# Optimization experiments

Hardware: AMD Instinct MI355X
Metric: run time of the kernel (lower is better)

## Reference

```python
import jax, jax.numpy as jnp
import numpy as np
from jax import lax

# ---- static config (R-C3D TEST cfg) ----
FEAT_STRIDE = 8
SCALES = np.array([2, 4, 5, 6, 8, 9, 10, 12, 14, 16], dtype=np.float32)
NUM_ANCHORS = SCALES.shape[0]  # A = 10
PRE_NMS_TOP_N = 6000
POST_NMS_TOP_N = 300
NMS_THRESH = 0.7
MIN_SIZE = 8.0


def _generate_anchors():
    # matches generate_anchors(base_size=feat_stride, scales): centered temporal windows
    ctr = (FEAT_STRIDE - 1) / 2.0
    ws = SCALES * FEAT_STRIDE
    return np.stack([ctr - 0.5 * (ws - 1.0), ctr + 0.5 * (ws - 1.0)], axis=1).astype(np.float32)  # [A,2]


def setup_inputs() -> dict:
    key = jax.random.key(0)
    k1, k2 = jax.random.split(key)
    B, L = 4, 4096
    scores_in = jax.random.normal(k1, (B, 2 * NUM_ANCHORS, L, 1, 1), dtype=jnp.float32)
    twin_deltas = jax.random.normal(k2, (B, 2 * NUM_ANCHORS, L, 1, 1), dtype=jnp.float32) * 0.1
    return {"scores_in": scores_in, "twin_deltas": twin_deltas}


def _iou_1d(twins):
    # twins: [N,2] inclusive temporal segments (torch-style +1 lengths)
    x1, x2 = twins[:, 0], twins[:, 1]
    length = x2 - x1 + 1.0
    inter = jnp.maximum(0.0, jnp.minimum(x2[:, None], x2[None, :]) - jnp.maximum(x1[:, None], x1[None, :]) + 1.0)
    union = length[:, None] + length[None, :] - inter
    return inter / union


def _nms_keep(iou, thresh):
    # greedy NMS on score-sorted candidates; keep[i] iff no earlier kept j overlaps > thresh
    N = iou.shape[0]
    idx = jnp.arange(N)
    def body(i, keep):
        suppressed = jnp.any(keep & (iou[:, i] > thresh) & (idx < i))
        return keep.at[i].set(~suppressed)
    return lax.fori_loop(0, N, body, jnp.zeros((N,), dtype=bool))


def _forward(scores_in, twin_deltas):
    B = scores_in.shape[0]
    A = NUM_ANCHORS
    L = scores_in.shape[2]
    anchors0 = jnp.asarray(_generate_anchors())  # [A,2]

    # objectness scores: second half of channels
    scores = scores_in[:, A:, :, :, :]  # [B,A,L,1,1]

    # shifted anchors, shift-major / anchor-minor to match (L,H,W,A) flattening
    shifts = jnp.arange(L, dtype=scores_in.dtype) * FEAT_STRIDE  # [L]
    anc = (anchors0[None, :, :] + shifts[:, None, None]).reshape(L * A, 2)  # [K*A,2]

    deltas = jnp.transpose(twin_deltas, (0, 2, 3, 4, 1)).reshape(B, -1, 2)  # [B,K*A,2]
    sc = jnp.transpose(scores, (0, 2, 3, 4, 1)).reshape(B, -1)  # [B,K*A]

    # twin_transform_inv
    widths = anc[:, 1] - anc[:, 0] + 1.0  # [K*A]
    ctr = anc[:, 0] + 0.5 * widths
    pred_ctr = deltas[:, :, 0] * widths[None, :] + ctr[None, :]
    pred_l = jnp.exp(deltas[:, :, 1]) * widths[None, :]
    proposals = jnp.stack([pred_ctr - 0.5 * pred_l, pred_ctr + 0.5 * pred_l], axis=-1)  # [B,K*A,2]

    # clip_twins to [0, L*feat_stride - 1]
    proposals = jnp.clip(proposals, 0.0, L * FEAT_STRIDE - 1.0)

    # filter: zero scores of too-short proposals
    ls = proposals[:, :, 1] - proposals[:, :, 0] + 1.0
    sc = jnp.where(ls < MIN_SIZE, 0.0, sc)

    # sort by score descending, take pre-NMS top-N
    order = jnp.argsort(-sc, axis=1)[:, :PRE_NMS_TOP_N]  # [B,P]
    prop_sorted = jnp.take_along_axis(proposals, order[:, :, None], axis=1)  # [B,P,2]

    def per_image(p):
        iou = _iou_1d(lax.stop_gradient(p))  # NMS decision is non-differentiable (layer propagates no grads via NMS)
        keep = _nms_keep(iou, NMS_THRESH)
        N = p.shape[0]
        # kept indices in sorted order, padded with N
        kept_idx = jnp.sort(jnp.where(keep, jnp.arange(N), N))[:POST_NMS_TOP_N]
        valid = kept_idx < N
        gi = jnp.minimum(kept_idx, N - 1)
        return jnp.where(valid[:, None], p[gi], 0.0)  # [post,2]

    props_out = jax.vmap(per_image)(prop_sorted)  # [B,post,2]
    batch_ids = jnp.broadcast_to(
        jnp.arange(B, dtype=scores_in.dtype)[:, None, None], (B, POST_NMS_TOP_N, 1)
    )
    return jnp.concatenate([batch_ids, props_out], axis=-1)  # [B,post,3]


def reference(scores_in, twin_deltas):
    return _forward(scores_in, twin_deltas)
```

## Files before the change

kernel.cpp:

```cpp
#include <hip/hip_runtime.h>
#include <stdint.h>

#pragma clang fp contract(off)

#define NA 10
#define LL 4096
#define NB 4
#define NSEL (LL * NA)
#define PRE2 2048
#define POST_NMS 300
#define CAND 4096
#define TWORDS 33792

__constant__ float c_WS[NA] = {16.f, 32.f, 40.f, 48.f, 64.f, 72.f, 80.f, 96.f, 112.f, 128.f};

__device__ inline void gload_lds16(const void* g, void* l) {
    __builtin_amdgcn_global_load_lds(
        (const __attribute__((address_space(1))) unsigned*)g,
        (__attribute__((address_space(3))) unsigned*)l, 16, 0, 0);
}

__global__ __launch_bounds__(1024, 1) void k_select(const float* __restrict__ scores,
                                                    const float* __restrict__ deltas,
                                                    unsigned long long* __restrict__ packed,
                                                    float2* __restrict__ prop,
                                                    unsigned long long* __restrict__ cand,
                                                    int* __restrict__ gcnt) {
    __shared__ unsigned hist[32768];
    __shared__ unsigned swsum[16];
    __shared__ unsigned sAfter;
    __shared__ int sSeg;
    __shared__ unsigned skmin;
    __shared__ int sCnt;

    const int tid = threadIdx.x;
    const int lane = tid & 63;
    const int wv = tid >> 6;
    const int b = blockIdx.x;

    if (tid == 0) sCnt = 0;
    {
        const uint4 z = make_uint4(0, 0, 0, 0);
        uint4* h4 = (uint4*)hist;
        #pragma unroll
        for (int i = 0; i < 8; ++i) h4[i * 1024 + tid] = z;
    }
    __syncthreads();

    {
        const float4* sRow = (const float4*)scores;
        const float4* dRow = (const float4*)deltas;
        float4 sc[2], da[2], db[2];
        #pragma unroll
        for (int pf = 0; pf < 2; ++pf) {
            sc[pf] = sRow[((b * 20 + 10 + pf) << 10) + tid];
            da[pf] = dRow[((b * 20 + 2 * pf) << 10) + tid];
            db[pf] = dRow[((b * 20 + 2 * pf + 1) << 10) + tid];
        }
        #pragma unroll
        for (int it = 0; it < 10; ++it) {
            const int cur = it & 1;
            const float4 s4 = sc[cur], d04 = da[cur], d14 = db[cur];
            if (it + 2 < 10) {
                sc[cur] = sRow[((b * 20 + 10 + it + 2) << 10) + tid];
                da[cur] = dRow[((b * 20 + 2 * (it + 2)) << 10) + tid];
                db[cur] = dRow[((b * 20 + 2 * (it + 2) + 1) << 10) + tid];
            }
            const float w = c_WS[it];
            const int l0 = tid << 2;
            const int r = (it << 12) + l0;
            unsigned key[4];
            float x1v[4], x2v[4];
            #pragma unroll
            for (int k = 0; k < 4; ++k) {
                const float d0 = (k == 0) ? d04.x : (k == 1) ? d04.y : (k == 2) ? d04.z : d04.w;
                const float d1 = (k == 0) ? d14.x : (k == 1) ? d14.y : (k == 2) ? d14.z : d14.w;
                float sv      = (k == 0) ? s4.x  : (k == 1) ? s4.y  : (k == 2) ? s4.z  : s4.w;
                const float ctr = (float)(8 * (l0 + k) + 4);
                const float pc = d0 * w + ctr;
                const float pl = expf(d1) * w;
                const float x1 = fminf(fmaxf(pc - 0.5f * pl, 0.0f), 32767.0f);
                const float x2 = fminf(fmaxf(pc + 0.5f * pl, 0.0f), 32767.0f);
                if (x2 - x1 + 1.0f < 8.0f) sv = 0.0f;
                const unsigned u = __float_as_uint(sv);
                key[k] = (u & 0x80000000u) ? ~u : (u | 0x80000000u);
                x1v[k] = x1; x2v[k] = x2;
            }
            unsigned long long p01[2], p23[2];
            #pragma unroll
            for (int k = 0; k < 4; ++k) {
                const unsigned long long pk = ((unsigned long long)key[k] << 32)
                    | (unsigned)(0xFFFFFFFFu - (unsigned)((l0 + k) * NA + it));
                if (k < 2) p01[k] = pk; else p23[k - 2] = pk;
            }
            *(ulonglong2*)&packed[b * NSEL + r]     = make_ulonglong2(p01[0], p01[1]);
            *(ulonglong2*)&packed[b * NSEL + r + 2] = make_ulonglong2(p23[0], p23[1]);
            *(float4*)&prop[b * NSEL + r]     = make_float4(x1v[0], x2v[0], x1v[1], x2v[1]);
            *(float4*)&prop[b * NSEL + r + 2] = make_float4(x1v[2], x2v[2], x1v[3], x2v[3]);
            #pragma unroll
            for (int k = 0; k < 4; ++k) {
                const unsigned kk = key[k] >> 16;
                atomicAdd(&hist[(((kk >> 1) & 31) << 10) | (kk >> 6)], 1u << ((kk & 1) << 4));
            }
        }
    }
    __syncthreads();

    unsigned s = 0;
    #pragma unroll
    for (int c = 0; c < 32; ++c) {
        const unsigned h = hist[(c << 10) + tid];
        s += (h & 0xFFFFu) + (h >> 16);
    }
    {
        unsigned inc = s;
        #pragma unroll
        for (int d = 1; d < 64; d <<= 1) {
            unsigned u = (unsigned)__shfl_down((int)inc, d, 64);
            if (lane + d < 64) inc += u;
        }
        if (lane == 0) swsum[wv] = inc;
        __syncthreads();
        if (tid < 16) {
            unsigned t = swsum[tid];
            unsigned winc = t;
            #pragma unroll
            for (int d = 1; d < 16; d <<= 1) {
                unsigned u = (unsigned)__shfl_down((int)winc, d, 64);
                if (tid + d < 16) winc += u;
            }
            swsum[tid] = winc - t;
        }
        __syncthreads();
        const unsigned glob = inc + swsum[wv];
        if (glob >= (unsigned)PRE2 && (glob - s) < (unsigned)PRE2) { sSeg = tid; sAfter = glob - s; }
    }
    __syncthreads();

    if (wv == 0) {
        const int seg = sSeg;
        const unsigned h = hist[((lane >> 1) << 10) + seg];
        const unsigned v = (lane & 1) ? (h >> 16) : (h & 0xFFFFu);
        unsigned inc = v;
        #pragma unroll
        for (int d = 1; d < 64; d <<= 1) {
            unsigned u = (unsigned)__shfl_down((int)inc, d, 64);
            if (lane + d < 64) inc += u;
        }
        const unsigned glob = inc + sAfter;
        if (glob >= (unsigned)PRE2 && (glob - v) < (unsigned)PRE2)
            skmin = ((unsigned)((seg << 6) + lane)) << 16;
    }
    __syncthreads();
    const unsigned kmin = skmin;

    const unsigned long long* pk = packed + b * NSEL;
    #pragma unroll
    for (int it = 0; it < NSEL / 2048; ++it) {
        const ulonglong2 pp = *(const ulonglong2*)&pk[(it * 1024 + tid) << 1];
        const bool pd0 = ((unsigned)(pp.x >> 32) >= kmin);
        const bool pd1 = ((unsigned)(pp.y >> 32) >= kmin);
        const unsigned long long m0 = __ballot(pd0);
        const unsigned long long m1 = __ballot(pd1);
        const int cnt = (int)(__popcll(m0) + __popcll(m1));
        int base = 0;
        if (cnt) {
            if (lane == 0) base = atomicAdd(&sCnt, cnt);
            base = __shfl(base, 0, 64);
            const unsigned long long below = (1ULL << lane) - 1ULL;
            if (pd0) {
                int pos = base + (int)__popcll(m0 & below);
                if (pos < CAND) cand[b * CAND + pos] = pp.x;
            }
            if (pd1) {
                int pos = base + (int)__popcll(m0) + (int)__popcll(m1 & below);
                if (pos < CAND) cand[b * CAND + pos] = pp.y;
            }
        }
    }
    __syncthreads();
    if (tid == 0) gcnt[b] = sCnt;
}

__global__ __launch_bounds__(256) void k_rank(const unsigned long long* __restrict__ cand,
                                              const int* __restrict__ gcnt,
                                              const float2* __restrict__ prop,
                                              float2* __restrict__ srt) {
    __shared__ __align__(16) unsigned long long keys[CAND];
    __shared__ unsigned part[4][64][4];

    const int b = blockIdx.y;
    const int n0 = gcnt[b];
    const int n = n0 < CAND ? n0 : CAND;
    const int ib = blockIdx.x * 256;
    if (ib >= n) return;

    const int tid = threadIdx.x;
    const int lane = tid & 63;
    const int wv = tid >> 6;
    const unsigned long long* cb = cand + b * CAND;

    const int nP = (n + 7) & ~7;
    for (int j = tid; j < nP; j += 256)
        keys[j] = (j < n) ? cb[j] : 0ULL;
    __syncthreads();

    const int i0 = ib + (lane << 2);
    const unsigned long long k0 = keys[i0 + 0];
    const unsigned long long k1 = keys[i0 + 1];
    const unsigned long long k2 = keys[i0 + 2];
    const unsigned long long k3 = keys[i0 + 3];

    const int q = nP >> 2;
    const ulonglong2* keys2 = (const ulonglong2*)keys;
    const int p0 = (wv * q) >> 1;
    const int pn = q >> 1;
    unsigned r0 = 0, r1 = 0, r2 = 0, r3 = 0;
    #pragma unroll 4
    for (int p = 0; p < pn; ++p) {
        ulonglong2 kj = keys2[p0 + p];
        r0 += (kj.x > k0); r0 += (kj.y > k0);
        r1 += (kj.x > k1); r1 += (kj.y > k1);
        r2 += (kj.x > k2); r2 += (kj.y > k2);
        r3 += (kj.x > k3); r3 += (kj.y > k3);
    }
    part[wv][lane][0] = r0; part[wv][lane][1] = r1;
    part[wv][lane][2] = r2; part[wv][lane][3] = r3;
    __syncthreads();

    const int ig = ib + tid;
    if (ig < n) {
        const int l_ = tid >> 2, c_ = tid & 3;
        unsigned r = part[0][l_][c_] + part[1][l_][c_] + part[2][l_][c_] + part[3][l_][c_];
        if (r < PRE2) {
            unsigned long long k = keys[ig];
            unsigned idx_ = 0xFFFFFFFFu - (unsigned)k;
            unsigned a_ = idx_ % 10u, l2_ = idx_ / 10u;
            srt[b * PRE2 + r] = prop[b * NSEL + (a_ << 12) + l2_];
        }
    }
}

__global__ __launch_bounds__(256) void k_mask(const float2* __restrict__ srt,
                                              unsigned long long* __restrict__ maskT) {
    const int g  = blockIdx.x;
    const int wj = blockIdx.y;
    const int b  = blockIdx.z;
    if (g * 4 > wj) return;

    __shared__ float2 lj[256];
    const int tid = threadIdx.x;
    lj[tid] = srt[b * PRE2 + (g << 8) + tid];
    __syncthreads();

    const int wi = (g << 2) + (tid >> 6);
    if (wi > wj) return;
    const int j = (wj << 6) + (tid & 63);

    float2 pj = srt[b * PRE2 + j];
    float ljn = pj.y - pj.x + 1.0f;
    unsigned long long bits = 0ULL;
    const int lbase = (tid >> 6) * 64;
    const int ibase = wi << 6;
    #pragma unroll 4
    for (int t = 0; t < 64; ++t) {
        float2 pv = lj[lbase + t];
        float inter = fminf(pj.y, pv.y) - fmaxf(pj.x, pv.x) + 1.0f;
        bool sup = false;
        if (inter > 0.0f) {
            float uni = ljn + (pv.y - pv.x + 1.0f) - inter;
            sup = (inter / uni) > 0.7f;
        }
        if ((ibase + t < j) && sup) bits |= (1ULL << t);
    }
    maskT[(size_t)b * TWORDS + (size_t)((wj * (wj + 1) / 2) + wi) * 64 + (tid & 63)] = bits;
}

__global__ __launch_bounds__(64, 1) void k_reduce(const unsigned long long* __restrict__ maskT,
                                                  const float2* __restrict__ srt,
                                                  float* __restrict__ out) {
    const int b = blockIdx.x;
    const int lane = threadIdx.x;
    __shared__ unsigned long long colbuf[4][2048];
    __shared__ unsigned long long Kl[32];
    __shared__ int sKl[POST_NMS];

    const unsigned long long* mTb = maskT + (size_t)b * TWORDS;

    auto stage = [&](int wv, int buf) {
        const char* src = (const char*)(mTb + (size_t)(wv * (wv + 1) / 2) * 64) + lane * 16;
        char* dst = (char*)(&colbuf[buf][0]);
        #pragma unroll
        for (int k = 0; k < 16; ++k)
            gload_lds16(src + k * 1024, dst + k * 1024);
    };

    stage(0, 0); stage(1, 1); stage(2, 2); stage(3, 3);

    int kept = 0;
    bool done = false;

    for (int w = 0; w < 32 && !done; ++w) {
        asm volatile("s_waitcnt vmcnt(48)" ::: "memory");
        __builtin_amdgcn_sched_barrier(0);

        const unsigned long long* cw = &colbuf[w & 3][0];
        unsigned long long SUP = 0ULL;
        for (int wi = 0; wi < w; ++wi)
            SUP |= Kl[wi] & cw[(wi << 6) + lane];
        unsigned long long x = cw[(w << 6) + lane];

        unsigned long long avail = ~__ballot(SUP != 0ULL);
        asm volatile("s_waitcnt lgkmcnt(0)" ::: "memory");
        __builtin_amdgcn_sched_barrier(0);
        asm volatile("" : "+v"(x));
        {
            int nx = w + 4;
            stage(nx < 31 ? nx : 31, nx & 3);
        }

        unsigned long long keptw = 0ULL;
        while (avail) {
            int j = __ffsll((long long)avail) - 1;
            if (lane == 0) sKl[kept] = (w << 6) + j;
            kept++; keptw |= (1ULL << j);
            if (kept >= POST_NMS) { done = true; break; }
            unsigned long long supb = __ballot(((x >> j) & 1ULL) != 0ULL);
            avail &= ~supb;
            avail &= ~(1ULL << j);
        }
        if (lane == 0) Kl[w] = keptw;
    }

    __syncthreads();
    for (int t = lane; t < POST_NMS; t += 64) {
        float x1 = 0.0f, x2 = 0.0f;
        if (t < kept) {
            float2 pv = srt[b * PRE2 + sKl[t]];
            x1 = pv.x; x2 = pv.y;
        }
        float* o = out + (size_t)(b * POST_NMS + t) * 3;
        o[0] = (float)b; o[1] = x1; o[2] = x2;
    }
}

extern "C" void kernel_launch(void* const* d_in, const int* in_sizes, int n_in,
                              void* d_out, int out_size, void* d_ws, size_t ws_size,
                              hipStream_t stream) {
    const float* scores = (const float*)d_in[0];
    const float* deltas = (const float*)d_in[1];
    float* out = (float*)d_out;

    char* ws = (char*)d_ws;
    unsigned long long* packed = (unsigned long long*)ws;
    float2* prop = (float2*)(ws + 1310720);
    float2* srt  = (float2*)(ws + 2621440);
    unsigned long long* maskT = (unsigned long long*)(ws + 2686976);
    unsigned long long* cand  = (unsigned long long*)(ws + 3768320);
    int* gcnt                 = (int*)(ws + 3899392);

    k_select<<<NB, 1024, 0, stream>>>(scores, deltas, packed, prop, cand, gcnt);
    k_rank<<<dim3(CAND / 256, NB), 256, 0, stream>>>(cand, gcnt, prop, srt);
    k_mask<<<dim3(8, 32, NB), 256, 0, stream>>>(srt, maskT);
    k_reduce<<<NB, 64, 0, stream>>>(maskT, srt, out);
}
```

Baseline: 87.33 us.

## Split proposal decode into a per-anchor grid kernel with partial histograms

Proposal decoding, packing and histogramming move out of the 4-block select kernel into a new kernel launched over (anchor, batch), 40 blocks in all. Each block builds a 4096-bin histogram from the top 12 key bits in shared memory and writes it out. The select kernel then sums the 10 partial histograms and finds the threshold bin in a single scan, replacing the two-level 16-bit search, and it also prefetches packed keys four iterations ahead. The aim is to use far more CUs for the decode phase. The cost is one extra launch and a coarser threshold bin, which lets more candidates pass and could approach the CAND capacity.

Result: faster. 77.80 us (-10.9%).

```diff
diff --git a/kernel.cpp b/kernel.cpp
--- a/kernel.cpp
+++ b/kernel.cpp
@@ -10,6 +10,7 @@
 #define PRE2 2048
 #define POST_NMS 300
 #define CAND 4096
+#define NHB12 4096
 #define TWORDS 33792
 
 __constant__ float c_WS[NA] = {16.f, 32.f, 40.f, 48.f, 64.f, 72.f, 80.f, 96.f, 112.f, 128.f};
@@ -20,16 +21,65 @@
         (__attribute__((address_space(3))) unsigned*)l, 16, 0, 0);
 }
 
-__global__ __launch_bounds__(1024, 1) void k_select(const float* __restrict__ scores,
-                                                    const float* __restrict__ deltas,
-                                                    unsigned long long* __restrict__ packed,
-                                                    float2* __restrict__ prop,
+__global__ __launch_bounds__(1024) void k_prep(const float* __restrict__ scores,
+                                               const float* __restrict__ deltas,
+                                               unsigned long long* __restrict__ packed,
+                                               float2* __restrict__ prop,
+                                               unsigned* __restrict__ hpart) {
+    __shared__ unsigned shist[NHB12];
+    const int tid = threadIdx.x;
+    const int a = blockIdx.x;
+    const int b = blockIdx.y;
+
+    #pragma unroll
+    for (int i = 0; i < 4; ++i) shist[i * 1024 + tid] = 0;
+    __syncthreads();
+
+    const float4 s4  = ((const float4*)scores)[((b * 20 + 10 + a) << 10) + tid];
+    const float4 d04 = ((const float4*)deltas)[((b * 20 + 2 * a) << 10) + tid];
+    const float4 d14 = ((const float4*)deltas)[((b * 20 + 2 * a + 1) << 10) + tid];
+    const float w = c_WS[a];
+    const int l0 = tid << 2;
+    const int r = (a << 12) + l0;
+
+    unsigned key[4];
+    float x1v[4], x2v[4];
+    #pragma unroll
+    for (int k = 0; k < 4; ++k) {
+        const float d0 = (k == 0) ? d04.x : (k == 1) ? d04.y : (k == 2) ? d04.z : d04.w;
+        const float d1 = (k == 0) ? d14.x : (k == 1) ? d14.y : (k == 2) ? d14.z : d14.w;
+        float sv      = (k == 0) ? s4.x  : (k == 1) ? s4.y  : (k == 2) ? s4.z  : s4.w;
+        const float ctr = (float)(8 * (l0 + k) + 4);
+        const float pc = d0 * w + ctr;
+        const float pl = expf(d1) * w;
+        const float x1 = fminf(fmaxf(pc - 0.5f * pl, 0.0f), 32767.0f);
+        const float x2 = fminf(fmaxf(pc + 0.5f * pl, 0.0f), 32767.0f);
+        if (x2 - x1 + 1.0f < 8.0f) sv = 0.0f;
+        const unsigned u = __float_as_uint(sv);
+        key[k] = (u & 0x80000000u) ? ~u : (u | 0x80000000u);
+        x1v[k] = x1; x2v[k] = x2;
+    }
+    const unsigned long long p0 = ((unsigned long long)key[0] << 32) | (unsigned)(0xFFFFFFFFu - (unsigned)((l0 + 0) * NA + a));
+    const unsigned long long p1 = ((unsigned long long)key[1] << 32) | (unsigned)(0xFFFFFFFFu - (unsigned)((l0 + 1) * NA + a));
+    const unsigned long long p2 = ((unsigned long long)key[2] << 32) | (unsigned)(0xFFFFFFFFu - (unsigned)((l0 + 2) * NA + a));
+    const unsigned long long p3 = ((unsigned long long)key[3] << 32) | (unsigned)(0xFFFFFFFFu - (unsigned)((l0 + 3) * NA + a));
+    *(ulonglong2*)&packed[b * NSEL + r]     = make_ulonglong2(p0, p1);
+    *(ulonglong2*)&packed[b * NSEL + r + 2] = make_ulonglong2(p2, p3);
+    *(float4*)&prop[b * NSEL + r]     = make_float4(x1v[0], x2v[0], x1v[1], x2v[1]);
+    *(float4*)&prop[b * NSEL + r + 2] = make_float4(x1v[2], x2v[2], x1v[3], x2v[3]);
+
+    #pragma unroll
+    for (int k = 0; k < 4; ++k) atomicAdd(&shist[key[k] >> 20], 1u);
+    __syncthreads();
+
+    ((uint4*)&hpart[(b * 10 + a) << 12])[tid] = ((const uint4*)shist)[tid];
+}
+
+__global__ __launch_bounds__(1024, 1) void k_select(const unsigned long long* __restrict__ packed,
+                                                    const unsigned* __restrict__ hpart,
                                                     unsigned long long* __restrict__ cand,
                                                     int* __restrict__ gcnt) {
-    __shared__ unsigned hist[32768];
     __shared__ unsigned swsum[16];
-    __shared__ unsigned sAfter;
-    __shared__ int sSeg;
     __shared__ unsigned skmin;
     __shared__ int sCnt;
 
@@ -39,125 +89,60 @@
     const int b = blockIdx.x;
 
     if (tid == 0) sCnt = 0;
+
+    uint4 h = make_uint4(0, 0, 0, 0);
+    #pragma unroll
+    for (int c = 0; c < 10; ++c) {
+        const uint4 v = ((const uint4*)hpart)[((b * 10 + c) << 10) + tid];
+        h.x += v.x; h.y += v.y; h.z += v.z; h.w += v.w;
+    }
+    const unsigned s = h.x + h.y + h.z + h.w;
+
+    unsigned inc = s;
+    #pragma unroll
+    for (int d = 1; d < 64; d <<= 1) {
+        unsigned u = (unsigned)__shfl_down((int)inc, d, 64);
+        if (lane + d < 64) inc += u;
+    }
+    if (lane == 0) swsum[wv] = inc;
+    __syncthreads();
+    if (tid < 16) {
+        unsigned t = swsum[tid];
+        unsigned winc = t;
+        #pragma unroll
+        for (int d = 1; d < 16; d <<= 1) {
+            unsigned u = (unsigned)__shfl_down((int)winc, d, 64);
+            if (tid + d < 16) winc += u;
+        }
+        swsum[tid] = winc - t;
+    }
+    __syncthreads();
+
     {
-        const uint4 z = make_uint4(0, 0, 0, 0);
-        uint4* h4 = (uint4*)hist;
-        #pragma unroll
-        for (int i = 0; i < 8; ++i) h4[i * 1024 + tid] = z;
-    }
-    __syncthreads();
-
-    {
-        const float4* sRow = (const float4*)scores;
-        const float4* dRow = (const float4*)deltas;
-        float4 sc[2], da[2], db[2];
-        #pragma unroll
-        for (int pf = 0; pf < 2; ++pf) {
-            sc[pf] = sRow[((b * 20 + 10 + pf) << 10) + tid];
-            da[pf] = dRow[((b * 20 + 2 * pf) << 10) + tid];
-            db[pf] = dRow[((b * 20 + 2 * pf + 1) << 10) + tid];
-        }
-        #pragma unroll
-        for (int it = 0; it < 10; ++it) {
-            const int cur = it & 1;
-            const float4 s4 = sc[cur], d04 = da[cur], d14 = db[cur];
-            if (it + 2 < 10) {
-                sc[cur] = sRow[((b * 20 + 10 + it + 2) << 10) + tid];
-                da[cur] = dRow[((b * 20 + 2 * (it + 2)) << 10) + tid];
-                db[cur] = dRow[((b * 20 + 2 * (it + 2) + 1) << 10) + tid];
-            }
-            const float w = c_WS[it];
-            const int l0 = tid << 2;
-            const int r = (it << 12) + l0;
-            unsigned key[4];
-            float x1v[4], x2v[4];
-            #pragma unroll
-            for (int k = 0; k < 4; ++k) {
-                const float d0 = (k == 0) ? d04.x : (k == 1) ? d04.y : (k == 2) ? d04.z : d04.w;
-                const float d1 = (k == 0) ? d14.x : (k == 1) ? d14.y : (k == 2) ? d14.z : d14.w;
-                float sv      = (k == 0) ? s4.x  : (k == 1) ? s4.y  : (k == 2) ? s4.z  : s4.w;
-                const float ctr = (float)(8 * (l0 + k) + 4);
-                const float pc = d0 * w + ctr;
-                const float pl = expf(d1) * w;
-                const float x1 = fminf(fmaxf(pc - 0.5f * pl, 0.0f), 32767.0f);
-                const float x2 = fminf(fmaxf(pc + 0.5f * pl, 0.0f), 32767.0f);
-                if (x2 - x1 + 1.0f < 8.0f) sv = 0.0f;
-                const unsigned u = __float_as_uint(sv);
-                key[k] = (u & 0x80000000u) ? ~u : (u | 0x80000000u);
-                x1v[k] = x1; x2v[k] = x2;
-            }
-            unsigned long long p01[2], p23[2];
-            #pragma unroll
-            for (int k = 0; k < 4; ++k) {
-                const unsigned long long pk = ((unsigned long long)key[k] << 32)
-                    | (unsigned)(0xFFFFFFFFu - (unsigned)((l0 + k) * NA + it));
-                if (k < 2) p01[k] = pk; else p23[k - 2] = pk;
-            }
-            *(ulonglong2*)&packed[b * NSEL + r]     = make_ulonglong2(p01[0], p01[1]);
-            *(ulonglong2*)&packed[b * NSEL + r + 2] = make_ulonglong2(p23[0], p23[1]);
-            *(float4*)&prop[b * NSEL + r]     = make_float4(x1v[0], x2v[0], x1v[1], x2v[1]);
-            *(float4*)&prop[b * NSEL + r + 2] = make_float4(x1v[2], x2v[2], x1v[3], x2v[3]);
-            #pragma unroll
-            for (int k = 0; k < 4; ++k) {
-                const unsigned kk = key[k] >> 16;
-                atomicAdd(&hist[(((kk >> 1) & 31) << 10) | (kk >> 6)], 1u << ((kk & 1) << 4));
-            }
-        }
-    }
-    __syncthreads();
-
-    unsigned s = 0;
-    #pragma unroll
-    for (int c = 0; c < 32; ++c) {
-        const unsigned h = hist[(c << 10) + tid];
-        s += (h & 0xFFFFu) + (h >> 16);
-    }
-    {
-        unsigned inc = s;
-        #pragma unroll
-        for (int d = 1; d < 64; d <<= 1) {
-            unsigned u = (unsigned)__shfl_down((int)inc, d, 64);
-            if (lane + d < 64) inc += u;
-        }
-        if (lane == 0) swsum[wv] = inc;
-        __syncthreads();
-        if (tid < 16) {
-            unsigned t = swsum[tid];
-            unsigned winc = t;
-            #pragma unroll
-            for (int d = 1; d < 16; d <<= 1) {
-                unsigned u = (unsigned)__shfl_down((int)winc, d, 64);
-                if (tid + d < 16) winc += u;
-            }
-            swsum[tid] = winc - t;
-        }
-        __syncthreads();
         const unsigned glob = inc + swsum[wv];
-        if (glob >= (unsigned)PRE2 && (glob - s) < (unsigned)PRE2) { sSeg = tid; sAfter = glob - s; }
-    }
-    __syncthreads();
-
-    if (wv == 0) {
-        const int seg = sSeg;
-        const unsigned h = hist[((lane >> 1) << 10) + seg];
-        const unsigned v = (lane & 1) ? (h >> 16) : (h & 0xFFFFu);
-        unsigned inc = v;
-        #pragma unroll
-        for (int d = 1; d < 64; d <<= 1) {
-            unsigned u = (unsigned)__shfl_down((int)inc, d, 64);
-            if (lane + d < 64) inc += u;
-        }
-        const unsigned glob = inc + sAfter;
-        if (glob >= (unsigned)PRE2 && (glob - v) < (unsigned)PRE2)
-            skmin = ((unsigned)((seg << 6) + lane)) << 16;
+        const unsigned base = glob - s;
+        const unsigned t3 = base + h.w;
+        const unsigned t2 = t3 + h.z;
+        const unsigned t1 = t2 + h.y;
+        const unsigned t0 = t1 + h.x;
+        const unsigned bx = (unsigned)(tid << 2);
+        if (t0 >= (unsigned)PRE2 && t0 - h.x < (unsigned)PRE2) skmin = (bx + 0) << 20;
+        if (t1 >= (unsigned)PRE2 && t1 - h.y < (unsigned)PRE2) skmin = (bx + 1) << 20;
+        if (t2 >= (unsigned)PRE2 && t2 - h.z < (unsigned)PRE2) skmin = (bx + 2) << 20;
+        if (t3 >= (unsigned)PRE2 && t3 - h.w < (unsigned)PRE2) skmin = (bx + 3) << 20;
     }
     __syncthreads();
     const unsigned kmin = skmin;
 
     const unsigned long long* pk = packed + b * NSEL;
+    ulonglong2 pf[4];
+    #pragma unroll
+    for (int i = 0; i < 4; ++i) pf[i] = *(const ulonglong2*)&pk[((i * 1024 + tid) << 1)];
     #pragma unroll
     for (int it = 0; it < NSEL / 2048; ++it) {
-        const ulonglong2 pp = *(const ulonglong2*)&pk[(it * 1024 + tid) << 1];
+        const ulonglong2 pp = pf[it & 3];
+        if (it + 4 < NSEL / 2048)
+            pf[it & 3] = *(const ulonglong2*)&pk[(((it + 4) * 1024 + tid) << 1)];
         const bool pd0 = ((unsigned)(pp.x >> 32) >= kmin);
         const bool pd1 = ((unsigned)(pp.y >> 32) >= kmin);
         const unsigned long long m0 = __ballot(pd0);
@@ -358,8 +343,10 @@
     unsigned long long* maskT = (unsigned long long*)(ws + 2686976);
     unsigned long long* cand  = (unsigned long long*)(ws + 3768320);
     int* gcnt                 = (int*)(ws + 3899392);
-
-    k_select<<<NB, 1024, 0, stream>>>(scores, deltas, packed, prop, cand, gcnt);
+    unsigned* hpart           = (unsigned*)(ws + 3899408);
+
+    k_prep<<<dim3(NA, NB), 1024, 0, stream>>>(scores, deltas, packed, prop, hpart);
+    k_select<<<NB, 1024, 0, stream>>>(packed, hpart, cand, gcnt);
     k_rank<<<dim3(CAND / 256, NB), 256, 0, stream>>>(cand, gcnt, prop, srt);
     k_mask<<<dim3(8, 32, NB), 256, 0, stream>>>(srt, maskT);
     k_reduce<<<NB, 64, 0, stream>>>(maskT, srt, out);
```
